# Optimization experiments

Hardware: AMD Instinct MI355X
Metric: run time of the kernel (lower is better)

Reference implementation:

```python
import jax, jax.numpy as jnp
import numpy as np

B, L, F = 64, 200, 64  # batch, max_route_len, link+route features

def setup_inputs() -> dict:
    key = jax.random.key(0)
    k1, k2 = jax.random.split(key)
    inp = jax.random.normal(k1, (B, L, L, F), dtype=jnp.float32)
    theta = jax.random.normal(k2, (L, L, F), dtype=jnp.float32)
    return {"input": inp, "theta": theta}

def reference(input, theta):
    # output[b,i,j] = input[b,i,j] . theta[i,j]  == per-position dot product
    return jnp.einsum('bijf,ijf->bij', input, theta)
```

## Files before the change

### kernel.cpp

```cpp
#include <hip/hip_runtime.h>


#define BQ 64
#define LQ 200
#define FQ 64
#define IJ (LQ * LQ)
#define EPB 16
#define CHUNKS (IJ / EPB)

typedef float f32x4 __attribute__((ext_vector_type(4)));

__global__ __launch_bounds__(256)
void IRLLinearModel_42786464203479_kernel(const float* __restrict__ inp,
                                          const float* __restrict__ theta,
                                          float* __restrict__ out) {
    const int chunk = blockIdx.x;

    const int g = threadIdx.x >> 4;
    const int s = threadIdx.x & 15;

    const int ij = chunk * EPB + g;

    const f32x4 t = *reinterpret_cast<const f32x4*>(theta + (size_t)ij * FQ + (size_t)s * 4);

    const float* in_base = inp + (size_t)ij * FQ + (size_t)s * 4;
    const size_t bstride = (size_t)IJ * FQ;

    float* out_base = out + ij;

    #pragma unroll 1
    for (int b0 = 0; b0 < BQ; b0 += 4) {
        const f32x4 a0 = __builtin_nontemporal_load(
            reinterpret_cast<const f32x4*>(in_base + (size_t)(b0 + 0) * bstride));
        const f32x4 a1 = __builtin_nontemporal_load(
            reinterpret_cast<const f32x4*>(in_base + (size_t)(b0 + 1) * bstride));
        const f32x4 a2 = __builtin_nontemporal_load(
            reinterpret_cast<const f32x4*>(in_base + (size_t)(b0 + 2) * bstride));
        const f32x4 a3 = __builtin_nontemporal_load(
            reinterpret_cast<const f32x4*>(in_base + (size_t)(b0 + 3) * bstride));

        float p0 = a0.x * t.x + a0.y * t.y + a0.z * t.z + a0.w * t.w;
        float p1 = a1.x * t.x + a1.y * t.y + a1.z * t.z + a1.w * t.w;
        float p2 = a2.x * t.x + a2.y * t.y + a2.z * t.z + a2.w * t.w;
        float p3 = a3.x * t.x + a3.y * t.y + a3.z * t.z + a3.w * t.w;

        p0 += __shfl_xor(p0, 1);  p1 += __shfl_xor(p1, 1);
        p2 += __shfl_xor(p2, 1);  p3 += __shfl_xor(p3, 1);
        p0 += __shfl_xor(p0, 2);  p1 += __shfl_xor(p1, 2);
        p2 += __shfl_xor(p2, 2);  p3 += __shfl_xor(p3, 2);
        p0 += __shfl_xor(p0, 4);  p1 += __shfl_xor(p1, 4);
        p2 += __shfl_xor(p2, 4);  p3 += __shfl_xor(p3, 4);
        p0 += __shfl_xor(p0, 8);  p1 += __shfl_xor(p1, 8);
        p2 += __shfl_xor(p2, 8);  p3 += __shfl_xor(p3, 8);

        if (s == 0) {
            __builtin_nontemporal_store(p0, out_base + (size_t)(b0 + 0) * IJ);
            __builtin_nontemporal_store(p1, out_base + (size_t)(b0 + 1) * IJ);
            __builtin_nontemporal_store(p2, out_base + (size_t)(b0 + 2) * IJ);
            __builtin_nontemporal_store(p3, out_base + (size_t)(b0 + 3) * IJ);
        }
    }
}

extern "C" void kernel_launch(void* const* d_in, const int* in_sizes, int n_in,
                              void* d_out, int out_size, void* d_ws, size_t ws_size,
                              hipStream_t stream) {
    const float* inp   = (const float*)d_in[0];
    const float* theta = (const float*)d_in[1];
    float* out = (float*)d_out;

    IRLLinearModel_42786464203479_kernel<<<CHUNKS, 256, 0, stream>>>(inp, theta, out);
}
```

Measured before the change: 135.5 us.

## Switch to persistent grid-stride loop over chunk-batch tiles

Replaces one block per 16-position chunk, which looped over all batches, with a fixed 2048-block grid that strides over (chunk, batch-group) tiles. This spreads the work more finely across blocks and aims to cut tail imbalance and improve memory-level parallelism. The trade-off is that theta is reloaded for every tile rather than once per chunk, adding cache traffic.

```diff
diff --git a/kernel.cpp b/kernel.cpp
--- a/kernel.cpp
+++ b/kernel.cpp
@@ -7,6 +7,8 @@
 #define IJ (LQ * LQ)
 #define EPB 16
 #define CHUNKS (IJ / EPB)
+#define TILES (CHUNKS * 16)
+#define GRID 2048
 
 typedef float f32x4 __attribute__((ext_vector_type(4)));
 
@@ -14,30 +16,31 @@
 void IRLLinearModel_42786464203479_kernel(const float* __restrict__ inp,
                                           const float* __restrict__ theta,
                                           float* __restrict__ out) {
-    const int chunk = blockIdx.x;
-
     const int g = threadIdx.x >> 4;
     const int s = threadIdx.x & 15;
-
-    const int ij = chunk * EPB + g;
-
-    const f32x4 t = *reinterpret_cast<const f32x4*>(theta + (size_t)ij * FQ + (size_t)s * 4);
-
-    const float* in_base = inp + (size_t)ij * FQ + (size_t)s * 4;
     const size_t bstride = (size_t)IJ * FQ;
 
-    float* out_base = out + ij;
+    #pragma unroll 1
+    for (int tile = blockIdx.x; tile < TILES; tile += GRID) {
+        const int chunk = tile >> 4;
+        const int b0    = (tile & 15) * 4;
 
-    #pragma unroll 1
-    for (int b0 = 0; b0 < BQ; b0 += 4) {
+        const int ij = chunk * EPB + g;
+
+        const f32x4 t = *reinterpret_cast<const f32x4*>(
+            theta + (size_t)ij * FQ + (size_t)s * 4);
+
+        const float* in_base = inp + (size_t)ij * FQ + (size_t)s * 4
+                                   + (size_t)b0 * bstride;
+
         const f32x4 a0 = __builtin_nontemporal_load(
-            reinterpret_cast<const f32x4*>(in_base + (size_t)(b0 + 0) * bstride));
+            reinterpret_cast<const f32x4*>(in_base + 0 * bstride));
         const f32x4 a1 = __builtin_nontemporal_load(
-            reinterpret_cast<const f32x4*>(in_base + (size_t)(b0 + 1) * bstride));
+            reinterpret_cast<const f32x4*>(in_base + 1 * bstride));
         const f32x4 a2 = __builtin_nontemporal_load(
-            reinterpret_cast<const f32x4*>(in_base + (size_t)(b0 + 2) * bstride));
+            reinterpret_cast<const f32x4*>(in_base + 2 * bstride));
         const f32x4 a3 = __builtin_nontemporal_load(
-            reinterpret_cast<const f32x4*>(in_base + (size_t)(b0 + 3) * bstride));
+            reinterpret_cast<const f32x4*>(in_base + 3 * bstride));
 
         float p0 = a0.x * t.x + a0.y * t.y + a0.z * t.z + a0.w * t.w;
         float p1 = a1.x * t.x + a1.y * t.y + a1.z * t.z + a1.w * t.w;
@@ -54,10 +57,11 @@
         p2 += __shfl_xor(p2, 8);  p3 += __shfl_xor(p3, 8);
 
         if (s == 0) {
-            __builtin_nontemporal_store(p0, out_base + (size_t)(b0 + 0) * IJ);
-            __builtin_nontemporal_store(p1, out_base + (size_t)(b0 + 1) * IJ);
-            __builtin_nontemporal_store(p2, out_base + (size_t)(b0 + 2) * IJ);
-            __builtin_nontemporal_store(p3, out_base + (size_t)(b0 + 3) * IJ);
+            float* ob = out + (size_t)b0 * IJ + ij;
+            __builtin_nontemporal_store(p0, ob + 0 * IJ);
+            __builtin_nontemporal_store(p1, ob + 1 * IJ);
+            __builtin_nontemporal_store(p2, ob + 2 * IJ);
+            __builtin_nontemporal_store(p3, ob + 3 * IJ);
         }
     }
 }
@@ -69,5 +73,5 @@
     const float* theta = (const float*)d_in[1];
     float* out = (float*)d_out;
 
-    IRLLinearModel_42786464203479_kernel<<<CHUNKS, 256, 0, stream>>>(inp, theta, out);
+    IRLLinearModel_42786464203479_kernel<<<GRID, 256, 0, stream>>>(inp, theta, out);
 }
```

Result: slower. 148.7 us (+9.8%).

## Software-pipeline batch loads and process two chunks per block

Applied to the files above, without the earlier changes.

Prefetches the next four batch rows of input before reducing the current four, so there are more loads in flight per thread. Each block now handles two position chunks in sequence, which halves the grid size. This aims to hide memory latency in a bandwidth-bound dot product, at the cost of more registers and fewer blocks for the scheduler to balance.

```diff
diff --git a/kernel.cpp b/kernel.cpp
--- a/kernel.cpp
+++ b/kernel.cpp
@@ -6,59 +6,74 @@
 #define FQ 64
 #define IJ (LQ * LQ)
 #define EPB 16
-#define CHUNKS (IJ / EPB)
+#define CPB 2
+#define GRID (IJ / (EPB * CPB))
 
 typedef float f32x4 __attribute__((ext_vector_type(4)));
+
+#define NTLOAD(p) __builtin_nontemporal_load(reinterpret_cast<const f32x4*>(p))
 
 __global__ __launch_bounds__(256)
 void IRLLinearModel_42786464203479_kernel(const float* __restrict__ inp,
                                           const float* __restrict__ theta,
                                           float* __restrict__ out) {
-    const int chunk = blockIdx.x;
-
     const int g = threadIdx.x >> 4;
     const int s = threadIdx.x & 15;
-
-    const int ij = chunk * EPB + g;
-
-    const f32x4 t = *reinterpret_cast<const f32x4*>(theta + (size_t)ij * FQ + (size_t)s * 4);
-
-    const float* in_base = inp + (size_t)ij * FQ + (size_t)s * 4;
     const size_t bstride = (size_t)IJ * FQ;
 
-    float* out_base = out + ij;
+    #pragma unroll 1
+    for (int c = 0; c < CPB; ++c) {
+        const int ij = (blockIdx.x * CPB + c) * EPB + g;
 
-    #pragma unroll 1
-    for (int b0 = 0; b0 < BQ; b0 += 4) {
-        const f32x4 a0 = __builtin_nontemporal_load(
-            reinterpret_cast<const f32x4*>(in_base + (size_t)(b0 + 0) * bstride));
-        const f32x4 a1 = __builtin_nontemporal_load(
-            reinterpret_cast<const f32x4*>(in_base + (size_t)(b0 + 1) * bstride));
-        const f32x4 a2 = __builtin_nontemporal_load(
-            reinterpret_cast<const f32x4*>(in_base + (size_t)(b0 + 2) * bstride));
-        const f32x4 a3 = __builtin_nontemporal_load(
-            reinterpret_cast<const f32x4*>(in_base + (size_t)(b0 + 3) * bstride));
+        const f32x4 t = *reinterpret_cast<const f32x4*>(
+            theta + (size_t)ij * FQ + (size_t)s * 4);
 
-        float p0 = a0.x * t.x + a0.y * t.y + a0.z * t.z + a0.w * t.w;
-        float p1 = a1.x * t.x + a1.y * t.y + a1.z * t.z + a1.w * t.w;
-        float p2 = a2.x * t.x + a2.y * t.y + a2.z * t.z + a2.w * t.w;
-        float p3 = a3.x * t.x + a3.y * t.y + a3.z * t.z + a3.w * t.w;
+        const float* in_base = inp + (size_t)ij * FQ + (size_t)s * 4;
+        float* ob = out + ij;
 
-        p0 += __shfl_xor(p0, 1);  p1 += __shfl_xor(p1, 1);
-        p2 += __shfl_xor(p2, 1);  p3 += __shfl_xor(p3, 1);
-        p0 += __shfl_xor(p0, 2);  p1 += __shfl_xor(p1, 2);
-        p2 += __shfl_xor(p2, 2);  p3 += __shfl_xor(p3, 2);
-        p0 += __shfl_xor(p0, 4);  p1 += __shfl_xor(p1, 4);
-        p2 += __shfl_xor(p2, 4);  p3 += __shfl_xor(p3, 4);
-        p0 += __shfl_xor(p0, 8);  p1 += __shfl_xor(p1, 8);
-        p2 += __shfl_xor(p2, 8);  p3 += __shfl_xor(p3, 8);
+        auto crunch = [&](const f32x4& a0, const f32x4& a1,
+                          const f32x4& a2, const f32x4& a3, int b0) {
+            float p0 = a0.x * t.x + a0.y * t.y + a0.z * t.z + a0.w * t.w;
+            float p1 = a1.x * t.x + a1.y * t.y + a1.z * t.z + a1.w * t.w;
+            float p2 = a2.x * t.x + a2.y * t.y + a2.z * t.z + a2.w * t.w;
+            float p3 = a3.x * t.x + a3.y * t.y + a3.z * t.z + a3.w * t.w;
 
-        if (s == 0) {
-            __builtin_nontemporal_store(p0, out_base + (size_t)(b0 + 0) * IJ);
-            __builtin_nontemporal_store(p1, out_base + (size_t)(b0 + 1) * IJ);
-            __builtin_nontemporal_store(p2, out_base + (size_t)(b0 + 2) * IJ);
-            __builtin_nontemporal_store(p3, out_base + (size_t)(b0 + 3) * IJ);
+            p0 += __shfl_xor(p0, 1);  p1 += __shfl_xor(p1, 1);
+            p2 += __shfl_xor(p2, 1);  p3 += __shfl_xor(p3, 1);
+            p0 += __shfl_xor(p0, 2);  p1 += __shfl_xor(p1, 2);
+            p2 += __shfl_xor(p2, 2);  p3 += __shfl_xor(p3, 2);
+            p0 += __shfl_xor(p0, 4);  p1 += __shfl_xor(p1, 4);
+            p2 += __shfl_xor(p2, 4);  p3 += __shfl_xor(p3, 4);
+            p0 += __shfl_xor(p0, 8);  p1 += __shfl_xor(p1, 8);
+            p2 += __shfl_xor(p2, 8);  p3 += __shfl_xor(p3, 8);
+
+            if (s == 0) {
+                __builtin_nontemporal_store(p0, ob + (size_t)(b0 + 0) * IJ);
+                __builtin_nontemporal_store(p1, ob + (size_t)(b0 + 1) * IJ);
+                __builtin_nontemporal_store(p2, ob + (size_t)(b0 + 2) * IJ);
+                __builtin_nontemporal_store(p3, ob + (size_t)(b0 + 3) * IJ);
+            }
+        };
+
+        f32x4 a0 = NTLOAD(in_base + 0 * bstride);
+        f32x4 a1 = NTLOAD(in_base + 1 * bstride);
+        f32x4 a2 = NTLOAD(in_base + 2 * bstride);
+        f32x4 a3 = NTLOAD(in_base + 3 * bstride);
+
+        #pragma unroll 1
+        for (int b0 = 0; b0 < BQ - 4; b0 += 4) {
+            const float* nb = in_base + (size_t)(b0 + 4) * bstride;
+            const f32x4 n0 = NTLOAD(nb + 0 * bstride);
+            const f32x4 n1 = NTLOAD(nb + 1 * bstride);
+            const f32x4 n2 = NTLOAD(nb + 2 * bstride);
+            const f32x4 n3 = NTLOAD(nb + 3 * bstride);
+
+            crunch(a0, a1, a2, a3, b0);
+
+            a0 = n0; a1 = n1; a2 = n2; a3 = n3;
         }
+
+        crunch(a0, a1, a2, a3, BQ - 4);
     }
 }
 
@@ -69,5 +84,5 @@
     const float* theta = (const float*)d_in[1];
     float* out = (float*)d_out;
 
-    IRLLinearModel_42786464203479_kernel<<<CHUNKS, 256, 0, stream>>>(inp, theta, out);
+    IRLLinearModel_42786464203479_kernel<<<GRID, 256, 0, stream>>>(inp, theta, out);
 }
```

Result: no change. 136.3 us (+0.7%).

## Remap grid so each block streams contiguous ij range for one batch

Applied to the files above, without the earlier changes.

Restructures the work split: instead of each block owning 16 positions and looping over all 64 batches (loading theta once), each block now owns one batch and a contiguous range of 100 chunks, streaming input and theta contiguously. This makes per-block input accesses sequential rather than strided by a full batch slice, which is meant to improve DRAM page locality. In exchange, theta is re-read once per batch (64x), relying on L2/MALL caching to absorb the extra traffic.

```diff
diff --git a/kernel.cpp b/kernel.cpp
--- a/kernel.cpp
+++ b/kernel.cpp
@@ -7,42 +7,53 @@
 #define IJ (LQ * LQ)
 #define EPB 16
 #define CHUNKS (IJ / EPB)
+#define RANGES 25
+#define CPR (CHUNKS / RANGES)
+#define GRID (RANGES * BQ)
 
 typedef float f32x4 __attribute__((ext_vector_type(4)));
+
+#define NTLOAD(p) __builtin_nontemporal_load(reinterpret_cast<const f32x4*>(p))
 
 __global__ __launch_bounds__(256)
 void IRLLinearModel_42786464203479_kernel(const float* __restrict__ inp,
                                           const float* __restrict__ theta,
                                           float* __restrict__ out) {
-    const int chunk = blockIdx.x;
+    const int r = blockIdx.x >> 6;
+    const int b = blockIdx.x & 63;
 
     const int g = threadIdx.x >> 4;
     const int s = threadIdx.x & 15;
 
-    const int ij = chunk * EPB + g;
+    const int chunk0 = r * CPR;
+    const size_t elem0 = (size_t)chunk0 * EPB + g;
 
-    const f32x4 t = *reinterpret_cast<const f32x4*>(theta + (size_t)ij * FQ + (size_t)s * 4);
+    const float* tb = theta + elem0 * FQ + (size_t)s * 4;
+    const float* ib = inp + (size_t)b * IJ * FQ + elem0 * FQ + (size_t)s * 4;
+    float* ob = out + (size_t)b * IJ + (size_t)chunk0 * EPB + g;
 
-    const float* in_base = inp + (size_t)ij * FQ + (size_t)s * 4;
-    const size_t bstride = (size_t)IJ * FQ;
-
-    float* out_base = out + ij;
+    const size_t cstep = (size_t)EPB * FQ;
 
     #pragma unroll 1
-    for (int b0 = 0; b0 < BQ; b0 += 4) {
-        const f32x4 a0 = __builtin_nontemporal_load(
-            reinterpret_cast<const f32x4*>(in_base + (size_t)(b0 + 0) * bstride));
-        const f32x4 a1 = __builtin_nontemporal_load(
-            reinterpret_cast<const f32x4*>(in_base + (size_t)(b0 + 1) * bstride));
-        const f32x4 a2 = __builtin_nontemporal_load(
-            reinterpret_cast<const f32x4*>(in_base + (size_t)(b0 + 2) * bstride));
-        const f32x4 a3 = __builtin_nontemporal_load(
-            reinterpret_cast<const f32x4*>(in_base + (size_t)(b0 + 3) * bstride));
+    for (int c = 0; c < CPR; c += 4) {
+        const size_t o0 = (size_t)(c + 0) * cstep;
+        const size_t o1 = (size_t)(c + 1) * cstep;
+        const size_t o2 = (size_t)(c + 2) * cstep;
+        const size_t o3 = (size_t)(c + 3) * cstep;
 
-        float p0 = a0.x * t.x + a0.y * t.y + a0.z * t.z + a0.w * t.w;
-        float p1 = a1.x * t.x + a1.y * t.y + a1.z * t.z + a1.w * t.w;
-        float p2 = a2.x * t.x + a2.y * t.y + a2.z * t.z + a2.w * t.w;
-        float p3 = a3.x * t.x + a3.y * t.y + a3.z * t.z + a3.w * t.w;
+        const f32x4 a0 = NTLOAD(ib + o0);
+        const f32x4 a1 = NTLOAD(ib + o1);
+        const f32x4 a2 = NTLOAD(ib + o2);
+        const f32x4 a3 = NTLOAD(ib + o3);
+        const f32x4 t0 = *reinterpret_cast<const f32x4*>(tb + o0);
+        const f32x4 t1 = *reinterpret_cast<const f32x4*>(tb + o1);
+        const f32x4 t2 = *reinterpret_cast<const f32x4*>(tb + o2);
+        const f32x4 t3 = *reinterpret_cast<const f32x4*>(tb + o3);
+
+        float p0 = a0.x * t0.x + a0.y * t0.y + a0.z * t0.z + a0.w * t0.w;
+        float p1 = a1.x * t1.x + a1.y * t1.y + a1.z * t1.z + a1.w * t1.w;
+        float p2 = a2.x * t2.x + a2.y * t2.y + a2.z * t2.z + a2.w * t2.w;
+        float p3 = a3.x * t3.x + a3.y * t3.y + a3.z * t3.z + a3.w * t3.w;
 
         p0 += __shfl_xor(p0, 1);  p1 += __shfl_xor(p1, 1);
         p2 += __shfl_xor(p2, 1);  p3 += __shfl_xor(p3, 1);
@@ -54,10 +65,10 @@
         p2 += __shfl_xor(p2, 8);  p3 += __shfl_xor(p3, 8);
 
         if (s == 0) {
-            __builtin_nontemporal_store(p0, out_base + (size_t)(b0 + 0) * IJ);
-            __builtin_nontemporal_store(p1, out_base + (size_t)(b0 + 1) * IJ);
-            __builtin_nontemporal_store(p2, out_base + (size_t)(b0 + 2) * IJ);
-            __builtin_nontemporal_store(p3, out_base + (size_t)(b0 + 3) * IJ);
+            __builtin_nontemporal_store(p0, ob + (size_t)(c + 0) * EPB);
+            __builtin_nontemporal_store(p1, ob + (size_t)(c + 1) * EPB);
+            __builtin_nontemporal_store(p2, ob + (size_t)(c + 2) * EPB);
+            __builtin_nontemporal_store(p3, ob + (size_t)(c + 3) * EPB);
         }
     }
 }
@@ -69,5 +80,5 @@
     const float* theta = (const float*)d_in[1];
     float* out = (float*)d_out;
 
-    IRLLinearModel_42786464203479_kernel<<<CHUNKS, 256, 0, stream>>>(inp, theta, out);
+    IRLLinearModel_42786464203479_kernel<<<GRID, 256, 0, stream>>>(inp, theta, out);
 }
```

New measurement: 168.3 us. 24.3% more time.
